# Optimization experiments

Hardware: AMD Instinct MI355X
Metric: run time of the kernel (lower is better)

Reference implementation:

```python
import jax, jax.numpy as jnp
import numpy as np

E = 1_000_000
NODE_IN = 64
EDGE_IN = 32
GLOBAL_IN = 32
HIDDEN = 128
EDGE_OUT = 32
B = 128


def setup_inputs() -> dict:
    key = jax.random.key(0)
    ks = jax.random.split(key, 10)
    src = jax.random.normal(ks[0], (E, NODE_IN), dtype=jnp.float32)
    dest = jax.random.normal(ks[1], (E, NODE_IN), dtype=jnp.float32)
    edge_attr = jax.random.normal(ks[2], (E, EDGE_IN), dtype=jnp.float32)
    u = jax.random.normal(ks[3], (B, GLOBAL_IN), dtype=jnp.float32)
    edge_batch = jnp.sort(jax.random.randint(ks[4], (E,), 0, B, dtype=jnp.int32)).astype(jnp.int64)
    in_dim = EDGE_IN + 2 * NODE_IN + GLOBAL_IN  # 192
    # Kaiming-uniform-ish init scale, values irrelevant for correctness baseline
    W1 = jax.random.normal(ks[5], (in_dim, HIDDEN), dtype=jnp.float32) * (1.0 / np.sqrt(in_dim))
    b1 = jnp.zeros((HIDDEN,), dtype=jnp.float32)
    W2 = jax.random.normal(ks[6], (HIDDEN, EDGE_OUT), dtype=jnp.float32) * (1.0 / np.sqrt(HIDDEN))
    b2 = jnp.zeros((EDGE_OUT,), dtype=jnp.float32)
    return {"src": src, "dest": dest, "edge_attr": edge_attr, "u": u,
            "edge_batch": edge_batch, "W1": W1, "b1": b1, "W2": W2, "b2": b2}


def reference(src, dest, edge_attr, u, edge_batch, W1, b1, W2, b2):
    # gather per-edge global features: [E, global_in_dim]
    u_expanded = u[edge_batch]
    # concat -> [E, edge_in + 2*node_in + global_in]
    combined = jnp.concatenate([src, dest, edge_attr, u_expanded], axis=1)
    # 2-layer MLP with ReLU
    h = jax.nn.relu(combined @ W1 + b1)
    out = h @ W2 + b2
    return out
```

## Files before the change

### kernel.cpp

```cpp
#include <hip/hip_runtime.h>

#define NODE_IN 64
#define EDGE_IN 32
#define GLOBAL_IN 32
#define HID 128
#define EOUT 32

typedef float f32x4 __attribute__((ext_vector_type(4)));
typedef float f32x2 __attribute__((ext_vector_type(2)));
typedef short s16x8 __attribute__((ext_vector_type(8)));
typedef unsigned short u16x8 __attribute__((ext_vector_type(8)));

#define XROW 384
#define HOFF 24576
#define LDSZ 40960

#define GLOADX4(dst, ptr) asm volatile("global_load_dwordx4 %0, %1, off" : "=v"(dst) : "v"(ptr))
#define GLOADD(dst, ptr)  asm volatile("global_load_dword %0, %1, off"   : "=v"(dst) : "v"(ptr))

__device__ __forceinline__ unsigned short f2bf(float f) {
  __bf16 h = (__bf16)f;
  return __builtin_bit_cast(unsigned short, h);
}

__device__ __forceinline__ s16x8 cvt8(f32x4 a, f32x4 b) {
  u16x8 v = { f2bf(a[0]), f2bf(a[1]), f2bf(a[2]), f2bf(a[3]),
              f2bf(b[0]), f2bf(b[1]), f2bf(b[2]), f2bf(b[3]) };
  return __builtin_bit_cast(s16x8, v);
}

__device__ __forceinline__ void bar_lds() {
  asm volatile("s_waitcnt lgkmcnt(0)" ::: "memory");
  __builtin_amdgcn_s_barrier();
  asm volatile("" ::: "memory");
}

__global__ __launch_bounds__(256) void edge_mlp(
    const float* __restrict__ srcp, const float* __restrict__ dstp,
    const float* __restrict__ eap, const float* __restrict__ up,
    const int* __restrict__ ebp, const float* __restrict__ W1,
    const float* __restrict__ b1, const float* __restrict__ W2,
    const float* __restrict__ b2, float* __restrict__ outp,
    int E, int ntiles)
{
  __shared__ __align__(16) char SM[LDSZ];

  const int t = threadIdx.x;
  const int wid = t >> 6;
  const int lane = t & 63;
  const int g = lane >> 4;
  const int r16 = lane & 15;
  const int rA = t >> 3, cA8 = (t & 7) * 8;
  const int rC = t >> 2, cC8 = (t & 3) * 8;
  const int Em1 = E - 1;

  s16x8 w1f[6][2];
#pragma unroll
  for (int kk = 0; kk < 6; ++kk) {
#pragma unroll
    for (int nt = 0; nt < 2; ++nt) {
      s16x8 v;
#pragma unroll
      for (int j = 0; j < 8; ++j)
        v[j] = (short)f2bf(W1[(32*kk + 8*g + j)*HID + 32*wid + 2*r16 + nt]);
      w1f[kk][nt] = v;
    }
  }
  s16x8 w2f[4][2];
#pragma unroll
  for (int kk = 0; kk < 4; ++kk) {
#pragma unroll
    for (int nt = 0; nt < 2; ++nt) {
      s16x8 v;
#pragma unroll
      for (int j = 0; j < 8; ++j)
        v[j] = (short)f2bf(W2[(32*kk + 8*g + j)*EOUT + 2*r16 + nt]);
      w2f[kk][nt] = v;
    }
  }
  const float b1v0 = b1[32*wid + 2*r16];
  const float b1v1 = b1[32*wid + 2*r16 + 1];
  const float b2v0 = b2[2*r16];
  const float b2v1 = b2[2*r16 + 1];

  f32x4 P0, P1, P2, P3, P4, P5, P6, P7, P8, P9, P10, P11;

  auto issue_gloads = [&](int mb, int eb) {
    const int r0 = min(mb + rA, Em1);
    const int r1 = min(mb + 32 + rA, Em1);
    const int r2 = min(mb + rC, Em1);
    const float* s0 = srcp + (size_t)r0 * NODE_IN + cA8;
    const float* s1 = srcp + (size_t)r1 * NODE_IN + cA8;
    const float* d0 = dstp + (size_t)r0 * NODE_IN + cA8;
    const float* d1 = dstp + (size_t)r1 * NODE_IN + cA8;
    const float* e0 = eap  + (size_t)r2 * EDGE_IN + cC8;
    const float* u0 = up   + (size_t)eb * GLOBAL_IN + cC8;
    GLOADX4(P0, s0);  GLOADX4(P1, s0 + 4);
    GLOADX4(P2, s1);  GLOADX4(P3, s1 + 4);
    GLOADX4(P4, d0);  GLOADX4(P5, d0 + 4);
    GLOADX4(P6, d1);  GLOADX4(P7, d1 + 4);
    GLOADX4(P8, e0);  GLOADX4(P9, e0 + 4);
    GLOADX4(P10, u0); GLOADX4(P11, u0 + 4);
  };

  const int sxw = (t & 7) ^ (rA & 7);
  const int sew = ((t & 3)     ) ^ (rC & 7);
  const int suw = (4 + (t & 3) ) ^ (rC & 7);
  auto write_x = [&]() {
    *(s16x8*)(SM + rA*XROW        + sxw*16)        = cvt8(P0, P1);
    *(s16x8*)(SM + (rA+32)*XROW   + sxw*16)        = cvt8(P2, P3);
    *(s16x8*)(SM + rA*XROW        + (8+sxw)*16)    = cvt8(P4, P5);
    *(s16x8*)(SM + (rA+32)*XROW   + (8+sxw)*16)    = cvt8(P6, P7);
    *(s16x8*)(SM + rC*XROW        + (16+sew)*16)   = cvt8(P8, P9);
    *(s16x8*)(SM + rC*XROW        + (16+suw)*16)   = cvt8(P10, P11);
  };

  int tile = blockIdx.x;
  const int TS = gridDim.x;
  int ebv;

  {
    const int eb0 = ebp[min(tile*64 + rC, Em1)];
    const int eb1 = ebp[min((tile + TS)*64 + rC, Em1)];
    issue_gloads(tile * 64, eb0);
    asm volatile("s_waitcnt vmcnt(0)" ::: "memory");
    __builtin_amdgcn_sched_barrier(0);
    write_x();
    issue_gloads((tile + TS) * 64, eb1);
    GLOADD(ebv, (ebp + min((tile + 2*TS)*64 + rC, Em1)));
  }
  bar_lds();

  for (; tile < ntiles; tile += TS) {
    const int mbase = tile * 64;

    f32x4 acc[4][2];
    {
      const f32x4 z = {0.f, 0.f, 0.f, 0.f};
#pragma unroll
      for (int mi = 0; mi < 4; ++mi) { acc[mi][0] = z; acc[mi][1] = z; }
    }
#pragma unroll
    for (int mi = 0; mi < 4; ++mi) {
      const int r = 16*mi + r16;
      const char* Rp = SM + r * XROW;
      const int s = r16 & 7;
      const s16x8 f0 = *(const s16x8*)(Rp + ((g     ^ s)      )*16);
      const s16x8 f1 = *(const s16x8*)(Rp + (((4+g) ^ s)      )*16);
      const s16x8 f2 = *(const s16x8*)(Rp + ((g     ^ s) +  8 )*16);
      const s16x8 f3 = *(const s16x8*)(Rp + (((4+g) ^ s) +  8 )*16);
      const s16x8 f4 = *(const s16x8*)(Rp + ((g     ^ s) + 16 )*16);
      const s16x8 f5 = *(const s16x8*)(Rp + (((4+g) ^ s) + 16 )*16);
      acc[mi][0] = __builtin_amdgcn_mfma_f32_16x16x32_bf16(f0, w1f[0][0], acc[mi][0], 0, 0, 0);
      acc[mi][1] = __builtin_amdgcn_mfma_f32_16x16x32_bf16(f0, w1f[0][1], acc[mi][1], 0, 0, 0);
      acc[mi][0] = __builtin_amdgcn_mfma_f32_16x16x32_bf16(f1, w1f[1][0], acc[mi][0], 0, 0, 0);
      acc[mi][1] = __builtin_amdgcn_mfma_f32_16x16x32_bf16(f1, w1f[1][1], acc[mi][1], 0, 0, 0);
      acc[mi][0] = __builtin_amdgcn_mfma_f32_16x16x32_bf16(f2, w1f[2][0], acc[mi][0], 0, 0, 0);
      acc[mi][1] = __builtin_amdgcn_mfma_f32_16x16x32_bf16(f2, w1f[2][1], acc[mi][1], 0, 0, 0);
      acc[mi][0] = __builtin_amdgcn_mfma_f32_16x16x32_bf16(f3, w1f[3][0], acc[mi][0], 0, 0, 0);
      acc[mi][1] = __builtin_amdgcn_mfma_f32_16x16x32_bf16(f3, w1f[3][1], acc[mi][1], 0, 0, 0);
      acc[mi][0] = __builtin_amdgcn_mfma_f32_16x16x32_bf16(f4, w1f[4][0], acc[mi][0], 0, 0, 0);
      acc[mi][1] = __builtin_amdgcn_mfma_f32_16x16x32_bf16(f4, w1f[4][1], acc[mi][1], 0, 0, 0);
      acc[mi][0] = __builtin_amdgcn_mfma_f32_16x16x32_bf16(f5, w1f[5][0], acc[mi][0], 0, 0, 0);
      acc[mi][1] = __builtin_amdgcn_mfma_f32_16x16x32_bf16(f5, w1f[5][1], acc[mi][1], 0, 0, 0);
    }

#pragma unroll
    for (int mi = 0; mi < 4; ++mi) {
#pragma unroll
      for (int j = 0; j < 4; ++j) {
        const float h0 = fmaxf(acc[mi][0][j] + b1v0, 0.f);
        const float h1 = fmaxf(acc[mi][1][j] + b1v1, 0.f);
        const unsigned int pk = (unsigned int)f2bf(h0) |
                                ((unsigned int)f2bf(h1) << 16);
        const int row = 16*mi + 4*g + j;
        const int ch = (4*wid + (r16 >> 2)) ^ ((4*g + j) & 7);
        *(unsigned int*)(SM + HOFF + row*256 + ch*16 + (r16 & 3)*4) = pk;
      }
    }
    bar_lds();

    asm volatile("s_waitcnt vmcnt(0)" ::: "memory");
    __builtin_amdgcn_sched_barrier(0);
    write_x();
    issue_gloads((tile + 2*TS) * 64, ebv);
    GLOADD(ebv, (ebp + min((tile + 3*TS)*64 + rC, Em1)));

    f32x4 acc2[2];
    {
      const f32x4 z = {0.f, 0.f, 0.f, 0.f};
      acc2[0] = z; acc2[1] = z;
    }
#pragma unroll
    for (int kk = 0; kk < 4; ++kk) {
      const int ch = (4*kk + g) ^ (r16 & 7);
      const s16x8 ah = *(const s16x8*)(SM + HOFF + (16*wid + r16)*256 + ch*16);
      acc2[0] = __builtin_amdgcn_mfma_f32_16x16x32_bf16(ah, w2f[kk][0], acc2[0], 0, 0, 0);
      acc2[1] = __builtin_amdgcn_mfma_f32_16x16x32_bf16(ah, w2f[kk][1], acc2[1], 0, 0, 0);
    }
#pragma unroll
    for (int j = 0; j < 4; ++j) {
      const int m = mbase + 16*wid + 4*g + j;
      if (m < E) {
        f32x2 o = { acc2[0][j] + b2v0, acc2[1][j] + b2v1 };
        *(f32x2*)(outp + (size_t)m*EOUT + 2*r16) = o;
      }
    }
    bar_lds();
  }
}

extern "C" void kernel_launch(void* const* d_in, const int* in_sizes, int n_in,
                              void* d_out, int out_size, void* d_ws, size_t ws_size,
                              hipStream_t stream) {
  const float* srcp = (const float*)d_in[0];
  const float* dstp = (const float*)d_in[1];
  const float* eap  = (const float*)d_in[2];
  const float* up   = (const float*)d_in[3];
  const int*   ebp  = (const int*)d_in[4];
  const float* W1   = (const float*)d_in[5];
  const float* b1   = (const float*)d_in[6];
  const float* W2   = (const float*)d_in[7];
  const float* b2   = (const float*)d_in[8];
  float* outp = (float*)d_out;

  const int E = in_sizes[0] / NODE_IN;
  const int ntiles = (E + 63) / 64;
  const int grid = ntiles < 2048 ? ntiles : 2048;

  edge_mlp<<<grid, 256, 0, stream>>>(srcp, dstp, eap, up, ebp, W1, b1, W2, b2,
                                     outp, E, ntiles);
}
```

Before: 159.0 us.

## Pre-pack bf16 weight fragments in a prep kernel and shrink persistent grid

Adds a small prep kernel that converts W1 and W2 to bf16 once and stores them in the workspace in MFMA fragment order. Each main-kernel block then loads its fragments with vector loads instead of doing many strided scalar fp32 loads and conversions. The persistent grid also shrinks from 2048 to 512 blocks, so per-block weight setup is amortised over more tiles. This costs an extra kernel launch and may lower the parallelism available to hide memory latency.

```diff
diff --git a/kernel.cpp b/kernel.cpp
--- a/kernel.cpp
+++ b/kernel.cpp
@@ -35,13 +35,32 @@
   asm volatile("" ::: "memory");
 }
 
+__global__ __launch_bounds__(64) void prep_w(const float* __restrict__ W1,
+                                             const float* __restrict__ W2,
+                                             unsigned short* __restrict__ wsf) {
+  const int f = blockIdx.x, l = threadIdx.x;
+  const int lg = l >> 4, lr = l & 15;
+  u16x8 v;
+  if (f < 48) {
+    const int kk = f >> 3, wd = (f >> 1) & 3, nt = f & 1;
+#pragma unroll
+    for (int j = 0; j < 8; ++j)
+      v[j] = f2bf(W1[(32*kk + 8*lg + j)*HID + 32*wd + 2*lr + nt]);
+  } else {
+    const int q = f - 48, kk = q >> 1, nt = q & 1;
+#pragma unroll
+    for (int j = 0; j < 8; ++j)
+      v[j] = f2bf(W2[(32*kk + 8*lg + j)*EOUT + 2*lr + nt]);
+  }
+  *(u16x8*)&wsf[f*512 + l*8] = v;
+}
+
 __global__ __launch_bounds__(256) void edge_mlp(
     const float* __restrict__ srcp, const float* __restrict__ dstp,
     const float* __restrict__ eap, const float* __restrict__ up,
-    const int* __restrict__ ebp, const float* __restrict__ W1,
-    const float* __restrict__ b1, const float* __restrict__ W2,
-    const float* __restrict__ b2, float* __restrict__ outp,
-    int E, int ntiles)
+    const int* __restrict__ ebp, const unsigned short* __restrict__ wsf,
+    const float* __restrict__ b1, const float* __restrict__ b2,
+    float* __restrict__ outp, int E, int ntiles)
 {
   __shared__ __align__(16) char SM[LDSZ];
 
@@ -57,26 +76,14 @@
   s16x8 w1f[6][2];
 #pragma unroll
   for (int kk = 0; kk < 6; ++kk) {
-#pragma unroll
-    for (int nt = 0; nt < 2; ++nt) {
-      s16x8 v;
-#pragma unroll
-      for (int j = 0; j < 8; ++j)
-        v[j] = (short)f2bf(W1[(32*kk + 8*g + j)*HID + 32*wid + 2*r16 + nt]);
-      w1f[kk][nt] = v;
-    }
+    w1f[kk][0] = *(const s16x8*)&wsf[(kk*8 + wid*2 + 0)*512 + lane*8];
+    w1f[kk][1] = *(const s16x8*)&wsf[(kk*8 + wid*2 + 1)*512 + lane*8];
   }
   s16x8 w2f[4][2];
 #pragma unroll
   for (int kk = 0; kk < 4; ++kk) {
-#pragma unroll
-    for (int nt = 0; nt < 2; ++nt) {
-      s16x8 v;
-#pragma unroll
-      for (int j = 0; j < 8; ++j)
-        v[j] = (short)f2bf(W2[(32*kk + 8*g + j)*EOUT + 2*r16 + nt]);
-      w2f[kk][nt] = v;
-    }
+    w2f[kk][0] = *(const s16x8*)&wsf[(48 + kk*2 + 0)*512 + lane*8];
+    w2f[kk][1] = *(const s16x8*)&wsf[(48 + kk*2 + 1)*512 + lane*8];
   }
   const float b1v0 = b1[32*wid + 2*r16];
   const float b1v1 = b1[32*wid + 2*r16 + 1];
@@ -223,11 +230,13 @@
   const float* W2   = (const float*)d_in[7];
   const float* b2   = (const float*)d_in[8];
   float* outp = (float*)d_out;
+  unsigned short* wsf = (unsigned short*)d_ws;
 
   const int E = in_sizes[0] / NODE_IN;
   const int ntiles = (E + 63) / 64;
-  const int grid = ntiles < 2048 ? ntiles : 2048;
-
-  edge_mlp<<<grid, 256, 0, stream>>>(srcp, dstp, eap, up, ebp, W1, b1, W2, b2,
+  const int grid = ntiles < 512 ? ntiles : 512;
+
+  prep_w<<<56, 64, 0, stream>>>(W1, W2, wsf);
+  edge_mlp<<<grid, 256, 0, stream>>>(srcp, dstp, eap, up, ebp, wsf, b1, b2,
                                      outp, E, ntiles);
 }
```

Result: slower. 162.2 us (+2.0%).
